# Performance work log

Measured on AMD Instinct MI355X. Metric: run time of the kernel, lower is better.

Reference implementation:

```python
import jax, jax.numpy as jnp
import numpy as np
import math

D = 256        # input_size == d_k == d_v (per the module: d_k = input_size)
H = 4          # n_heads
MAX_LEN = 800  # PositionalEncoding max_len
NEG = float(-(2**32) + 1)
LN_EPS = 1e-5


def _make_pe():
    pe = np.zeros((MAX_LEN, D), dtype=np.float32)
    pos = np.arange(MAX_LEN, dtype=np.float32)[:, None]
    div = np.exp(np.arange(0, D, 2, dtype=np.float32) * -(math.log(10000.0) / D))
    pe[:, 0::2] = np.sin(pos * div)
    pe[:, 1::2] = np.cos(pos * div)
    return jnp.asarray(pe)


def setup_inputs() -> dict:
    key = jax.random.key(0)
    ks = jax.random.split(key, 12)
    B, L = 32, 512

    def xavier(k, shape):
        fan_in, fan_out = shape[0], shape[1]
        std = math.sqrt(2.0 / (fan_in + fan_out))
        return jax.random.normal(k, shape, dtype=jnp.float32) * std

    return {
        "Q": jax.random.normal(ks[0], (B, L, D), dtype=jnp.float32),
        "K": jax.random.normal(ks[1], (B, L, D), dtype=jnp.float32),
        "V": jax.random.normal(ks[2], (B, L, D), dtype=jnp.float32),
        "mask": jax.random.randint(ks[3], (B, L), 0, 2).astype(jnp.bool_),
        "pe": _make_pe(),
        "W_q": xavier(ks[4], (D, H * D)),
        "W_k": xavier(ks[5], (D, H * D)),
        "W_v": xavier(ks[6], (D, H * D)),
        "W_o": xavier(ks[7], (H * D, D)),
        "w1": xavier(ks[8], (D, D)),
        "b1": jnp.zeros((D,), dtype=jnp.float32),
        "w2": xavier(ks[9], (D, D)),
        "b2": jnp.zeros((D,), dtype=jnp.float32),
        "gamma": jnp.ones((D,), dtype=jnp.float32),
        "beta": jnp.zeros((D,), dtype=jnp.float32),
    }


def _layer_norm(x, gamma, beta):
    mu = jnp.mean(x, axis=-1, keepdims=True)
    var = jnp.mean(jnp.square(x - mu), axis=-1, keepdims=True)
    return (x - mu) * jax.lax.rsqrt(var + LN_EPS) * gamma + beta


def _mha(Q, K, V, mask, W_q, W_k, W_v, W_o):
    B, Lq, _ = Q.shape
    Lk = K.shape[1]

    def split_heads(X, W, L):
        # (B, L, D) @ (D, H*D) -> (B*H, L, D)
        return (X @ W).reshape(B, L, H, D).transpose(0, 2, 1, 3).reshape(B * H, L, D)

    Qh = split_heads(Q, W_q, Lq)
    Kh = split_heads(K, W_k, Lk)
    Vh = split_heads(V, W_v, Lk)

    scale = D ** 0.5 + 1e-6
    scores = jnp.einsum('bqd,bkd->bqk', Qh, Kh) / scale  # (B*H, Lq, Lk)

    pad = jnp.broadcast_to(mask[:, None, :], (B, H, Lq)).reshape(B * H, Lq)
    pad_mask = jnp.broadcast_to(pad[:, :, None], (B * H, Lq, Lk))
    causal = jnp.triu(jnp.ones((Lq, Lk), dtype=jnp.bool_), k=1)
    full_mask = causal[None] | pad_mask
    scores = jnp.where(full_mask, NEG, scores)

    att = jax.nn.softmax(scores, axis=-1)
    Vatt = jnp.einsum('bqk,bkd->bqd', att, Vh)  # (B*H, Lq, D)
    Vatt = Vatt.reshape(B, H, Lq, D).transpose(0, 2, 1, 3).reshape(B, Lq, H * D)
    return Vatt @ W_o


def reference(Q, K, V, mask, pe, W_q, W_k, W_v, W_o, w1, b1, w2, b2, gamma, beta):
    Lq, Lk, Lv = Q.shape[1], K.shape[1], V.shape[1]
    Qp = Q + pe[None, :Lq]
    Kp = K + pe[None, :Lk]
    Vp = V + pe[None, :Lv]

    Vatt = _mha(Qp, Kp, Vp, mask, W_q, W_k, W_v, W_o)
    X = _layer_norm(Qp + Vatt, gamma, beta)
    ffn = jax.nn.relu(X @ w1.T + b1) @ w2.T + b2
    return _layer_norm(ffn + X, gamma, beta)
```

## Files before the change

kernel.cpp:

```cpp
#include <hip/hip_runtime.h>
#include <stdint.h>

#define SEQ   512
#define DM    256
#define NB    32
#define NH    4
#define HD    (NH * DM)
#define PE_MASK (SEQ * DM - 1)
#define NEGV  (-4294967295.0f)

typedef __attribute__((ext_vector_type(8))) short short8;
typedef __attribute__((ext_vector_type(4))) float f32x4;

#if defined(__has_builtin)
#if __has_builtin(__builtin_amdgcn_global_load_lds)
#define HAS_ASYNC 1
#endif
#endif
#ifndef HAS_ASYNC
#define HAS_ASYNC 0
#endif

__device__ __forceinline__ float b2f(unsigned short u) {
    return __uint_as_float(((uint32_t)u) << 16);
}
__device__ __forceinline__ unsigned short f2b(float f) {
    uint32_t u = __float_as_uint(f);
    u += 0x7fffu + ((u >> 16) & 1u);
    return (unsigned short)(u >> 16);
}

__global__ __launch_bounds__(256) void mask_canon(
    const unsigned char* __restrict__ raw, int* __restrict__ canon)
{
    __shared__ int enc_byte, enc_odd;
    int tid = threadIdx.x;
    if (tid == 0) { enc_byte = 0; enc_odd = 0; }
    __syncthreads();
    if (tid < 255 && raw[tid * 4 + 1]) atomicOr(&enc_byte, 1);
    if (tid < 128 && ((const int*)raw)[tid * 2 + 1]) atomicOr(&enc_odd, 1);
    __syncthreads();
    int i = blockIdx.x * 256 + tid;
    int v;
    if (enc_byte)      v = (raw[i] != 0);
    else if (enc_odd)  v = (((const int*)raw)[i] != 0);
    else               v = ((((const int*)raw)[i * 2] | ((const int*)raw)[i * 2 + 1]) != 0);
    canon[i] = v;
}

__global__ __launch_bounds__(256) void addpe3(
    const float* __restrict__ Q, const float* __restrict__ K,
    const float* __restrict__ V, const float* __restrict__ pe,
    unsigned short* __restrict__ Qp, unsigned short* __restrict__ Kp,
    unsigned short* __restrict__ Vp)
{
    int blk = blockIdx.x;
    int seg = blk >> 12;
    const float* X = (seg == 0) ? Q : (seg == 1) ? K : V;
    unsigned short* O = (seg == 0) ? Qp : (seg == 1) ? Kp : Vp;
    long i = (long)((blk & 4095) * 256 + threadIdx.x) * 4;
    float4 x = *reinterpret_cast<const float4*>(X + i);
    float4 p = *reinterpret_cast<const float4*>(pe + (i & PE_MASK));
    ushort4 o;
    o.x = f2b(x.x + p.x); o.y = f2b(x.y + p.y);
    o.z = f2b(x.z + p.z); o.w = f2b(x.w + p.w);
    *reinterpret_cast<ushort4*>(O + i) = o;
}

__global__ __launch_bounds__(256) void conv2(
    const float* __restrict__ w1, const float* __restrict__ w2,
    unsigned short* __restrict__ o1, unsigned short* __restrict__ o2)
{
    int blk = blockIdx.x;
    const float* in = (blk < 64) ? w1 : w2;
    unsigned short* out = (blk < 64) ? o1 : o2;
    long i = (long)((blk & 63) * 256 + threadIdx.x) * 4;
    float4 x = *reinterpret_cast<const float4*>(in + i);
    ushort4 o;
    o.x = f2b(x.x); o.y = f2b(x.y); o.z = f2b(x.z); o.w = f2b(x.w);
    *reinterpret_cast<ushort4*>(out + i) = o;
}

__global__ __launch_bounds__(256) void transpose_f2b3(
    const float* __restrict__ in0, const float* __restrict__ in1,
    const float* __restrict__ in2, unsigned short* __restrict__ out,
    int ldin, int ldout, long outStride)
{
    int z = blockIdx.z;
    const float* in = (z == 0) ? in0 : (z == 1) ? in1 : in2;
    unsigned short* op = out + z * outStride;
    __shared__ unsigned short tile[32][33];
    int r0 = blockIdx.y * 32, c0 = blockIdx.x * 32;
    int i = threadIdx.x >> 3;
    int j = (threadIdx.x & 7) * 4;
    float4 v = *reinterpret_cast<const float4*>(in + (long)(r0 + i) * ldin + c0 + j);
    tile[i][j + 0] = f2b(v.x); tile[i][j + 1] = f2b(v.y);
    tile[i][j + 2] = f2b(v.z); tile[i][j + 3] = f2b(v.w);
    __syncthreads();
    ushort4 w;
    w.x = tile[j + 0][i]; w.y = tile[j + 1][i]; w.z = tile[j + 2][i]; w.w = tile[j + 3][i];
    *reinterpret_cast<ushort4*>(op + (long)(c0 + i) * ldout + r0 + j) = w;
}

__global__ __launch_bounds__(256) void transpose_f2b(
    const float* __restrict__ in, unsigned short* __restrict__ out,
    int ldin, int ldout)
{
    __shared__ unsigned short tile[32][33];
    int r0 = blockIdx.y * 32, c0 = blockIdx.x * 32;
    int i = threadIdx.x >> 3;
    int j = (threadIdx.x & 7) * 4;
    float4 v = *reinterpret_cast<const float4*>(in + (long)(r0 + i) * ldin + c0 + j);
    tile[i][j + 0] = f2b(v.x); tile[i][j + 1] = f2b(v.y);
    tile[i][j + 2] = f2b(v.z); tile[i][j + 3] = f2b(v.w);
    __syncthreads();
    ushort4 w;
    w.x = tile[j + 0][i]; w.y = tile[j + 1][i]; w.z = tile[j + 2][i]; w.w = tile[j + 3][i];
    *reinterpret_cast<ushort4*>(out + (long)(c0 + i) * ldout + r0 + j) = w;
}

__global__ __launch_bounds__(256) void transpose_bf16(
    const unsigned short* __restrict__ in, unsigned short* __restrict__ out,
    int ldin, int ldout, long sInB, long sInH, long sOutB, long sOutH, int Hdiv)
{
    int z = blockIdx.z; int b = z / Hdiv; int h = z % Hdiv;
    const unsigned short* ip = in + b * sInB + h * sInH;
    unsigned short* op = out + b * sOutB + h * sOutH;
    __shared__ unsigned short tile[32][33];
    int r0 = blockIdx.y * 32, c0 = blockIdx.x * 32;
    int i = threadIdx.x >> 3;
    int j = (threadIdx.x & 7) * 4;
    ushort4 v = *reinterpret_cast<const ushort4*>(ip + (long)(r0 + i) * ldin + c0 + j);
    tile[i][j + 0] = v.x; tile[i][j + 1] = v.y; tile[i][j + 2] = v.z; tile[i][j + 3] = v.w;
    __syncthreads();
    ushort4 w;
    w.x = tile[j + 0][i]; w.y = tile[j + 1][i]; w.z = tile[j + 2][i]; w.w = tile[j + 3][i];
    *reinterpret_cast<ushort4*>(op + (long)(c0 + i) * ldout + r0 + j) = w;
}

__global__ __launch_bounds__(256) void vmean_part(
    const unsigned short* __restrict__ Vh, float* __restrict__ part)
{
    int bl = blockIdx.x, seg = blockIdx.y;
    const unsigned short* p = Vh + (long)bl * SEQ * HD + (long)seg * 64 * HD;
    int c = threadIdx.x * 4;
    float s0 = 0.f, s1 = 0.f, s2 = 0.f, s3 = 0.f;
    for (int l = 0; l < 64; ++l) {
        ushort4 v = *reinterpret_cast<const ushort4*>(p + (long)l * HD + c);
        s0 += b2f(v.x); s1 += b2f(v.y); s2 += b2f(v.z); s3 += b2f(v.w);
    }
    float4 o = {s0, s1, s2, s3};
    *reinterpret_cast<float4*>(part + (long)(bl * 8 + seg) * HD + c) = o;
}

__global__ __launch_bounds__(256) void vmean_reduce(
    const float* __restrict__ part, unsigned short* __restrict__ Vm)
{
    int bl = blockIdx.x;
    int c = threadIdx.x * 4;
    const float* p = part + (long)bl * 8 * HD + c;
    float s0 = 0.f, s1 = 0.f, s2 = 0.f, s3 = 0.f;
#pragma unroll
    for (int seg = 0; seg < 8; ++seg) {
        float4 v = *reinterpret_cast<const float4*>(p + (long)seg * HD);
        s0 += v.x; s1 += v.y; s2 += v.z; s3 += v.w;
    }
    const float inv = 1.0f / SEQ;
    ushort4 o;
    o.x = f2b(s0 * inv); o.y = f2b(s1 * inv);
    o.z = f2b(s2 * inv); o.w = f2b(s3 * inv);
    *reinterpret_cast<ushort4*>(Vm + (long)bl * HD + c) = o;
}

__global__ __launch_bounds__(256) void fix_mask(
    const unsigned short* __restrict__ Vm, unsigned short* __restrict__ Vatt,
    const int* __restrict__ maskc, int b0)
{
    int row = blockIdx.x;
    int bl = row >> 9, l = row & (SEQ - 1);
    if (maskc[(long)(b0 + bl) * SEQ + l] == 0) return;
    int c = threadIdx.x * 4;
    ushort4 v = *reinterpret_cast<const ushort4*>(Vm + (long)bl * HD + c);
    *reinterpret_cast<ushort4*>(Vatt + (long)row * HD + c) = v;
}

template<bool BIAS, bool RELU, bool OUTBF16>
__global__ __launch_bounds__(256) void gemm_bt(
    const unsigned short* __restrict__ A, int lda,
    const unsigned short* __restrict__ B, int ldb,
    void* __restrict__ Cv, int ldc,
    const float* __restrict__ bias, float scale, int K, int Hdiv,
    long sAb, long sAh, long sAz,
    long sBb, long sBh, long sBz,
    long sCb, long sCh, long sCz)
{
    const int m0 = blockIdx.y * 128;
    const int n0 = blockIdx.x * 128;
    int z  = blockIdx.z;
    int bb = z / Hdiv, hh = z % Hdiv;
    const unsigned short* Ab = A + bb * sAb + hh * sAh + (long)z * sAz;
    const unsigned short* Bb = B + bb * sBb + hh * sBh + (long)z * sBz;
    long coff = bb * sCb + hh * sCh + (long)z * sCz;

    __shared__ unsigned short As[128 * 32];
    __shared__ unsigned short Bs[128 * 32];

    const int tid  = threadIdx.x;
    const int lane = tid & 63;
    const int wave = tid >> 6;
    const int wm   = (wave >> 1) * 64;
    const int wn   = (wave & 1) * 64;
    const int lm   = lane & 15;
    const int kq   = (lane >> 4) * 8;

    f32x4 acc[4][4] = {};

    for (int k0 = 0; k0 < K; k0 += 32) {
#pragma unroll
        for (int it = 0; it < 2; ++it) {
            int id = tid + it * 256;
            int r  = id >> 2;
            int c8 = (id & 3) * 8;
            const unsigned short* gA = Ab + (long)(m0 + r) * lda + k0 + c8;
            const unsigned short* gB = Bb + (long)(n0 + r) * ldb + k0 + c8;
#if HAS_ASYNC
            unsigned short* lA = &As[(size_t)(it * 256 + wave * 64) * 8];
            unsigned short* lB = &Bs[(size_t)(it * 256 + wave * 64) * 8];
            __builtin_amdgcn_global_load_lds(
                (const __attribute__((address_space(1))) void*)gA,
                (__attribute__((address_space(3))) void*)lA, 16, 0, 0);
            __builtin_amdgcn_global_load_lds(
                (const __attribute__((address_space(1))) void*)gB,
                (__attribute__((address_space(3))) void*)lB, 16, 0, 0);
#else
            *reinterpret_cast<uint4*>(&As[(size_t)id * 8]) =
                *reinterpret_cast<const uint4*>(gA);
            *reinterpret_cast<uint4*>(&Bs[(size_t)id * 8]) =
                *reinterpret_cast<const uint4*>(gB);
#endif
        }
        __syncthreads();

        short8 af[4], bfr[4];
#pragma unroll
        for (int i = 0; i < 4; ++i)
            af[i] = *reinterpret_cast<const short8*>(&As[(wm + i * 16 + lm) * 32 + kq]);
#pragma unroll
        for (int j = 0; j < 4; ++j)
            bfr[j] = *reinterpret_cast<const short8*>(&Bs[(wn + j * 16 + lm) * 32 + kq]);
#pragma unroll
        for (int i = 0; i < 4; ++i)
#pragma unroll
            for (int j = 0; j < 4; ++j)
                acc[i][j] = __builtin_amdgcn_mfma_f32_16x16x32_bf16(af[i], bfr[j], acc[i][j], 0, 0, 0);
        __syncthreads();
    }

#pragma unroll
    for (int j = 0; j < 4; ++j) {
        int col  = n0 + wn + j * 16 + lm;
        float bv = 0.f;
        if (BIAS) bv = bias[col];
#pragma unroll
        for (int i = 0; i < 4; ++i) {
#pragma unroll
            for (int r = 0; r < 4; ++r) {
                int row = m0 + wm + i * 16 + (lane >> 4) * 4 + r;
                float v = acc[i][j][r] * scale + bv;
                if (RELU) v = fmaxf(v, 0.f);
                long idx = coff + (long)row * ldc + col;
                if (OUTBF16) reinterpret_cast<unsigned short*>(Cv)[idx] = f2b(v);
                else         reinterpret_cast<float*>(Cv)[idx] = v;
            }
        }
    }
}

__global__ __launch_bounds__(256, 2) void flash_attn(
    const unsigned short* __restrict__ Qh,
    const unsigned short* __restrict__ Kh,
    const unsigned short* __restrict__ VhT,
    unsigned short* __restrict__ Vatt,
    const int* __restrict__ maskc, int bh0, float scale, int nbh)
{
    const int tid  = threadIdx.x;
    const int lane = tid & 63;
    const int wave = tid >> 6;
    const int lm   = lane & 15;
    const int qg   = lane >> 4;
    const int kq   = qg * 8;

    const int L = blockIdx.x;
    int z, qt;
    if ((nbh & 7) == 0) {
        int x = L & 7, m = L >> 3;
        qt = m & 7;
        z  = x + 8 * (m >> 3);
    } else {
        z = L % nbh; qt = L / nbh;
    }
    const int b_l = z >> 2, h = z & 3;
    const int m0  = qt * 64;
    const int wq0 = m0 + wave * 16;
    const long qkbase = (long)b_l * SEQ * HD + (long)h * DM;
    const unsigned short* Aq = Qh + qkbase;
    const unsigned short* Ak = Kh + qkbase;
    const unsigned short* Av = VhT + (long)b_l * SEQ * HD + (long)h * SEQ * DM;
    unsigned short* Ov = Vatt + qkbase;
    const int bglob = (bh0 + z) >> 2;

    __shared__ unsigned short Ks[SEQ * 32];
    __shared__ __align__(16) unsigned short Pw[4][16][40];

    f32x4 S[32] = {};
    const int NT = (m0 >> 4) + wave + 1;

    for (int kc = 0; kc < 8; ++kc) {
        for (int it = 0; it <= qt; ++it) {
            int id = tid + it * 256;
            const unsigned short* g = Ak + (long)(id >> 2) * HD + kc * 32 + (id & 3) * 8;
#if HAS_ASYNC
            unsigned short* l = &Ks[(size_t)(it * 256 + wave * 64) * 8];
            __builtin_amdgcn_global_load_lds(
                (const __attribute__((address_space(1))) void*)g,
                (__attribute__((address_space(3))) void*)l, 16, 0, 0);
#else
            *reinterpret_cast<uint4*>(&Ks[(size_t)id * 8]) =
                *reinterpret_cast<const uint4*>(g);
#endif
        }
        short8 qf = *reinterpret_cast<const short8*>(
            Aq + (long)(wq0 + lm) * HD + kc * 32 + kq);
        __syncthreads();
#pragma unroll
        for (int nt = 0; nt < 32; ++nt) {
            if (nt < NT) {
                short8 bf = *reinterpret_cast<const short8*>(&Ks[(nt * 16 + lm) * 32 + kq]);
                S[nt] = __builtin_amdgcn_mfma_f32_16x16x32_bf16(qf, bf, S[nt], 0, 0, 0);
            }
        }
        __syncthreads();
    }

    unsigned short* Vb0 = Ks;
    unsigned short* Vb1 = Ks + 8192;
#pragma unroll
    for (int it = 0; it < 4; ++it) {
        int id = tid + it * 256;
        const unsigned short* g = Av + (long)(id >> 2) * SEQ + (id & 3) * 8;
#if HAS_ASYNC
        unsigned short* l = &Vb0[(size_t)(it * 256 + wave * 64) * 8];
        __builtin_amdgcn_global_load_lds(
            (const __attribute__((address_space(1))) void*)g,
            (__attribute__((address_space(3))) void*)l, 16, 0, 0);
#else
        *reinterpret_cast<uint4*>(&Vb0[(size_t)id * 8]) =
            *reinterpret_cast<const uint4*>(g);
#endif
    }

    int   qrow[4];
    bool  rowm[4];
    float mx[4], sm[4];
#pragma unroll
    for (int r = 0; r < 4; ++r) {
        int q = wq0 + qg * 4 + r;
        qrow[r] = q;
        rowm[r] = maskc[bglob * SEQ + q] != 0;
        mx[r] = -3.4e38f;
    }
#pragma unroll
    for (int nt = 0; nt < 32; ++nt) {
        int k = nt * 16 + lm;
#pragma unroll
        for (int r = 0; r < 4; ++r) {
            float v = S[nt][r] * scale;
            if (k > qrow[r]) v = NEGV;
            S[nt][r] = v;
            mx[r] = fmaxf(mx[r], v);
        }
    }
#pragma unroll
    for (int r = 0; r < 4; ++r) {
#pragma unroll
        for (int off = 8; off >= 1; off >>= 1)
            mx[r] = fmaxf(mx[r], __shfl_xor(mx[r], off));
        sm[r] = 0.f;
    }
    uint32_t pk[32][2];
#pragma unroll
    for (int nt = 0; nt < 32; ++nt) {
        float e0 = __expf(S[nt][0] - mx[0]);
        float e1 = __expf(S[nt][1] - mx[1]);
        float e2 = __expf(S[nt][2] - mx[2]);
        float e3 = __expf(S[nt][3] - mx[3]);
        sm[0] += e0; sm[1] += e1; sm[2] += e2; sm[3] += e3;
        pk[nt][0] = (uint32_t)f2b(e0) | ((uint32_t)f2b(e1) << 16);
        pk[nt][1] = (uint32_t)f2b(e2) | ((uint32_t)f2b(e3) << 16);
    }
#pragma unroll
    for (int r = 0; r < 4; ++r) {
#pragma unroll
        for (int off = 8; off >= 1; off >>= 1)
            sm[r] += __shfl_xor(sm[r], off);
        sm[r] = 1.0f / sm[r];
    }

    const int KC = 2 * (qt + 1);
    f32x4 O[16] = {};
#pragma unroll
    for (int kc2 = 0; kc2 < 16; ++kc2) {
        if (kc2 < KC) {
            unsigned short* Vcur = (kc2 & 1) ? Vb1 : Vb0;
            __syncthreads();
            if (kc2 + 1 < KC) {
                unsigned short* Vnext = (kc2 & 1) ? Vb0 : Vb1;
#pragma unroll
                for (int it = 0; it < 4; ++it) {
                    int id = tid + it * 256;
                    const unsigned short* g =
                        Av + (long)(id >> 2) * SEQ + (kc2 + 1) * 32 + (id & 3) * 8;
#if HAS_ASYNC
                    unsigned short* l = &Vnext[(size_t)(it * 256 + wave * 64) * 8];
                    __builtin_amdgcn_global_load_lds(
                        (const __attribute__((address_space(1))) void*)g,
                        (__attribute__((address_space(3))) void*)l, 16, 0, 0);
#else
                    *reinterpret_cast<uint4*>(&Vnext[(size_t)id * 8]) =
                        *reinterpret_cast<const uint4*>(g);
#endif
                }
            }
#pragma unroll
            for (int t = 0; t < 2; ++t) {
                int nt = kc2 * 2 + t;
#pragma unroll
                for (int r = 0; r < 4; ++r)
                    Pw[wave][qg * 4 + r][t * 16 + lm] =
                        (unsigned short)(pk[nt][r >> 1] >> ((r & 1) * 16));
            }
            short8 pf = *reinterpret_cast<const short8*>(&Pw[wave][lm][kq]);
#pragma unroll
            for (int nt2 = 0; nt2 < 16; ++nt2) {
                short8 vf = *reinterpret_cast<const short8*>(&Vcur[(nt2 * 16 + lm) * 32 + kq]);
                O[nt2] = __builtin_amdgcn_mfma_f32_16x16x32_bf16(pf, vf, O[nt2], 0, 0, 0);
            }
        }
    }

#pragma unroll
    for (int nt2 = 0; nt2 < 16; ++nt2) {
#pragma unroll
        for (int r = 0; r < 4; ++r) {
            if (!rowm[r]) {
                int l = wq0 + qg * 4 + r;
                Ov[(long)l * HD + nt2 * 16 + lm] = f2b(O[nt2][r] * sm[r]);
            }
        }
    }
}

__global__ __launch_bounds__(256) void ln1_kernel(
    const unsigned short* __restrict__ AttO, const float* __restrict__ Q,
    const float* __restrict__ pe,
    const float* __restrict__ gamma, const float* __restrict__ beta,
    float* __restrict__ outf, unsigned short* __restrict__ outb)
{
    int row  = blockIdx.x * 4 + (threadIdx.x >> 6);
    int lane = threadIdx.x & 63;
    long base = (long)row * DM + lane * 4;
    ushort4 a = *reinterpret_cast<const ushort4*>(AttO + base);
    float4 qv = *reinterpret_cast<const float4*>(Q + base);
    float4 pv = *reinterpret_cast<const float4*>(pe + (base & PE_MASK));
    float x[4] = {b2f(a.x) + qv.x + pv.x, b2f(a.y) + qv.y + pv.y,
                  b2f(a.z) + qv.z + pv.z, b2f(a.w) + qv.w + pv.w};
    float s = x[0] + x[1] + x[2] + x[3];
#pragma unroll
    for (int off = 32; off > 0; off >>= 1) s += __shfl_xor(s, off);
    float mu = s * (1.0f / DM);
    float vs = 0.f;
#pragma unroll
    for (int t = 0; t < 4; ++t) { float d = x[t] - mu; vs += d * d; }
#pragma unroll
    for (int off = 32; off > 0; off >>= 1) vs += __shfl_xor(vs, off);
    float inv = rsqrtf(vs * (1.0f / DM) + 1e-5f);
    int d0 = lane * 4;
    float4 g = *reinterpret_cast<const float4*>(gamma + d0);
    float4 bt = *reinterpret_cast<const float4*>(beta + d0);
    float4 o;
    o.x = (x[0] - mu) * inv * g.x + bt.x;
    o.y = (x[1] - mu) * inv * g.y + bt.y;
    o.z = (x[2] - mu) * inv * g.z + bt.z;
    o.w = (x[3] - mu) * inv * g.w + bt.w;
    *reinterpret_cast<float4*>(outf + base) = o;
    ushort4 ob;
    ob.x = f2b(o.x); ob.y = f2b(o.y); ob.z = f2b(o.z); ob.w = f2b(o.w);
    *reinterpret_cast<ushort4*>(outb + base) = ob;
}

__global__ __launch_bounds__(256) void ln2_kernel(
    const float* __restrict__ F, const float* __restrict__ X,
    const float* __restrict__ gamma, const float* __restrict__ beta,
    float* __restrict__ out)
{
    int row  = blockIdx.x * 4 + (threadIdx.x >> 6);
    int lane = threadIdx.x & 63;
    long base = (long)row * DM + lane * 4;
    float4 a = *reinterpret_cast<const float4*>(F + base);
    float4 c = *reinterpret_cast<const float4*>(X + base);
    float x[4] = {a.x + c.x, a.y + c.y, a.z + c.z, a.w + c.w};
    float s = x[0] + x[1] + x[2] + x[3];
#pragma unroll
    for (int off = 32; off > 0; off >>= 1) s += __shfl_xor(s, off);
    float mu = s * (1.0f / DM);
    float vs = 0.f;
#pragma unroll
    for (int t = 0; t < 4; ++t) { float d = x[t] - mu; vs += d * d; }
#pragma unroll
    for (int off = 32; off > 0; off >>= 1) vs += __shfl_xor(vs, off);
    float inv = rsqrtf(vs * (1.0f / DM) + 1e-5f);
    int d0 = lane * 4;
    float4 g = *reinterpret_cast<const float4*>(gamma + d0);
    float4 bt = *reinterpret_cast<const float4*>(beta + d0);
    float4 o;
    o.x = (x[0] - mu) * inv * g.x + bt.x;
    o.y = (x[1] - mu) * inv * g.y + bt.y;
    o.z = (x[2] - mu) * inv * g.z + bt.z;
    o.w = (x[3] - mu) * inv * g.w + bt.w;
    *reinterpret_cast<float4*>(out + base) = o;
}

extern "C" void kernel_launch(void* const* d_in, const int* in_sizes, int n_in,
                              void* d_out, int out_size, void* d_ws, size_t ws_size,
                              hipStream_t stream)
{
    const float* Q  = (const float*)d_in[0];
    const float* Ki = (const float*)d_in[1];
    const float* Vi = (const float*)d_in[2];
    const unsigned char* mask_raw = (const unsigned char*)d_in[3];
    const float* pe = (const float*)d_in[4];
    const float* Wq = (const float*)d_in[5];
    const float* Wk = (const float*)d_in[6];
    const float* Wv = (const float*)d_in[7];
    const float* Wo = (const float*)d_in[8];
    const float* w1 = (const float*)d_in[9];
    const float* b1 = (const float*)d_in[10];
    const float* w2 = (const float*)d_in[11];
    const float* b2 = (const float*)d_in[12];
    const float* gamma = (const float*)d_in[13];
    const float* beta  = (const float*)d_in[14];
    float* out = (float*)d_out;

    const size_t MiB = 1048576;
    char* ws = (char*)d_ws;

    int CB = 1;
    for (int cb = 32; cb >= 1; cb >>= 1) {
        size_t scr_sz = (size_t)(5 * cb) * MiB + (size_t)cb * 34816;
        if (scr_sz < 24 * MiB) scr_sz = 24 * MiB;
        if ((59 * MiB + scr_sz) <= ws_size) { CB = cb; break; }
    }
    const int NCH = NB / CB;

    unsigned short* WqT  = (unsigned short*)(ws);
    unsigned short* WkT  = WqT + 262144;
    unsigned short* WvT  = WkT + 262144;
    unsigned short* WoT  = WvT + 262144;
    unsigned short* w1b  = (unsigned short*)(ws + 2 * MiB);
    unsigned short* w2b  = w1b + 65536;
    int*            maskc = (int*)(ws + 2 * MiB + 262144);
    unsigned short* Qp   = (unsigned short*)(ws + 3 * MiB);
    unsigned short* Kp   = (unsigned short*)(ws + 11 * MiB);
    unsigned short* Vp   = (unsigned short*)(ws + 19 * MiB);
    unsigned short* AttO = (unsigned short*)(ws + 27 * MiB);
    unsigned short* Xb   = (unsigned short*)(ws + 35 * MiB);
    float*          Xf   = (float*)(ws + 43 * MiB);
    char*           scr  = ws + 59 * MiB;
    unsigned short* Qh   = (unsigned short*)(scr);
    unsigned short* Kh   = (unsigned short*)(scr + (size_t)CB * MiB);
    unsigned short* Vh   = (unsigned short*)(scr + (size_t)2 * CB * MiB);
    unsigned short* VhT  = (unsigned short*)(scr + (size_t)3 * CB * MiB);
    unsigned short* Vatt = (unsigned short*)(scr + (size_t)4 * CB * MiB);
    float*          part = (float*)(scr + (size_t)5 * CB * MiB);
    unsigned short* Vm   = (unsigned short*)(scr + (size_t)5 * CB * MiB
                                             + (size_t)CB * 8 * HD * 4);
    unsigned short* H1   = (unsigned short*)(scr);
    float*          Ff   = (float*)(scr + 8 * MiB);

    const float scale = (float)(1.0 / (16.0 + 1e-6));
    const long CROWS = (long)CB * SEQ;
    const long CBELT = (long)CB * MiB / 2;

    mask_canon<<<64, 256, 0, stream>>>(mask_raw, maskc);
    transpose_f2b3<<<dim3(32, 8, 3), 256, 0, stream>>>(Wq, Wk, Wv, WqT, HD, DM, 262144);
    transpose_f2b<<<dim3(8, 32, 1), 256, 0, stream>>>(Wo, WoT, DM, HD);
    conv2<<<128, 256, 0, stream>>>(w1, w2, w1b, w2b);
    addpe3<<<12288, 256, 0, stream>>>(Q, Ki, Vi, pe, Qp, Kp, Vp);

    for (int c = 0; c < NCH; ++c) {
        const long r0   = (long)c * CROWS;
        const int  bh0  = c * CB * NH;
        const int  gy   = (int)(CROWS / 128);
        const int  nbh  = CB * NH;

        gemm_bt<false, false, true><<<dim3(8, gy, 3), 256, 0, stream>>>(
            Qp + r0 * DM, DM, WqT, DM, Qh, HD, nullptr, 1.f, DM,
            1, 4194304, 0, 0, 262144, 0, 0, CBELT, 0, 0);

        transpose_bf16<<<dim3(8, 16, CB * NH), 256, 0, stream>>>(
            Vh, VhT, HD, SEQ, (long)SEQ * HD, DM, (long)SEQ * HD, (long)SEQ * DM, NH);

        vmean_part<<<dim3(CB, 8), 256, 0, stream>>>(Vh, part);
        vmean_reduce<<<CB, 256, 0, stream>>>(part, Vm);

        flash_attn<<<dim3(8 * nbh, 1, 1), 256, 0, stream>>>(
            Qh, Kh, VhT, Vatt, maskc, bh0, scale, nbh);

        fix_mask<<<(int)CROWS, 256, 0, stream>>>(Vm, Vatt, maskc, c * CB);

        gemm_bt<false, false, true><<<dim3(2, gy, 1), 256, 0, stream>>>(
            Vatt, HD, WoT, HD, AttO + r0 * DM, DM, nullptr, 1.f, HD,
            1, 0,0,0, 0,0,0, 0,0,0);
    }

    ln1_kernel<<<4096, 256, 0, stream>>>(AttO, Q, pe, gamma, beta, Xf, Xb);

    gemm_bt<true, true, true><<<dim3(2, 128, 1), 256, 0, stream>>>(
        Xb, DM, w1b, DM, H1, DM, b1, 1.f, DM, 1, 0,0,0, 0,0,0, 0,0,0);
    gemm_bt<true, false, false><<<dim3(2, 128, 1), 256, 0, stream>>>(
        H1, DM, w2b, DM, Ff, DM, b2, 1.f, DM, 1, 0,0,0, 0,0,0, 0,0,0);

    ln2_kernel<<<4096, 256, 0, stream>>>(Ff, Xf, gamma, beta, out);
}
```

Measured before the change: 351.5 us.

## Double-buffer K tiles with XOR-swizzled LDS layout in flash attention

The K-chunk staging in the attention kernel now uses two LDS buffers, so the next 32-column K slice is prefetched while MFMAs consume the current one. The first V chunk is also issued during the last K iteration. K and V tiles are stored with an XOR swizzle to cut LDS bank conflicts on fragment reads. In exchange, shared memory doubles to 64KB for K, which may limit occupancy. The kernel also now stages all 512 K rows on every tile instead of only the causally needed ones, so early query tiles do more global traffic.

New measurement: 348.1 us. No clear change (-1.0%).

```diff
diff --git a/kernel.cpp b/kernel.cpp
--- a/kernel.cpp
+++ b/kernel.cpp
@@ -28,6 +28,10 @@
     uint32_t u = __float_as_uint(f);
     u += 0x7fffu + ((u >> 16) & 1u);
     return (unsigned short)(u >> 16);
+}
+
+__device__ __forceinline__ int swzb(int b) {
+    return b ^ (((b >> 7) & 7) << 4);
 }
 
 __global__ __launch_bounds__(256) void mask_canon(
@@ -276,6 +280,50 @@
     }
 }
 
+__device__ __forceinline__ void stage_k32(
+    unsigned short* __restrict__ buf, const unsigned short* __restrict__ Ak,
+    int kc, int tid, int wave)
+{
+#pragma unroll
+    for (int it = 0; it < 8; ++it) {
+        int id = tid + it * 256;
+#if HAS_ASYNC
+        int U = swzb(id * 16);
+        const unsigned short* g = Ak + (long)(U >> 6) * HD + kc * 32 + ((U >> 4) & 3) * 8;
+        unsigned short* l = buf + (size_t)(it * 256 + wave * 64) * 8;
+        __builtin_amdgcn_global_load_lds(
+            (const __attribute__((address_space(1))) void*)g,
+            (__attribute__((address_space(3))) void*)l, 16, 0, 0);
+#else
+        const unsigned short* g = Ak + (long)(id >> 2) * HD + kc * 32 + (id & 3) * 8;
+        *reinterpret_cast<uint4*>((char*)buf + swzb(id * 16)) =
+            *reinterpret_cast<const uint4*>(g);
+#endif
+    }
+}
+
+__device__ __forceinline__ void stage_v32(
+    unsigned short* __restrict__ buf, const unsigned short* __restrict__ Av,
+    int chunk, int tid, int wave)
+{
+#pragma unroll
+    for (int it = 0; it < 4; ++it) {
+        int id = tid + it * 256;
+#if HAS_ASYNC
+        int U = swzb(id * 16);
+        const unsigned short* g = Av + (long)(U >> 6) * SEQ + chunk * 32 + ((U >> 4) & 3) * 8;
+        unsigned short* l = buf + (size_t)(it * 256 + wave * 64) * 8;
+        __builtin_amdgcn_global_load_lds(
+            (const __attribute__((address_space(1))) void*)g,
+            (__attribute__((address_space(3))) void*)l, 16, 0, 0);
+#else
+        const unsigned short* g = Av + (long)(id >> 2) * SEQ + chunk * 32 + (id & 3) * 8;
+        *reinterpret_cast<uint4*>((char*)buf + swzb(id * 16)) =
+            *reinterpret_cast<const uint4*>(g);
+#endif
+    }
+}
+
 __global__ __launch_bounds__(256, 2) void flash_attn(
     const unsigned short* __restrict__ Qh,
     const unsigned short* __restrict__ Kh,
@@ -309,54 +357,34 @@
     unsigned short* Ov = Vatt + qkbase;
     const int bglob = (bh0 + z) >> 2;
 
-    __shared__ unsigned short Ks[SEQ * 32];
+    __shared__ unsigned short Ks[2 * SEQ * 32];
     __shared__ __align__(16) unsigned short Pw[4][16][40];
 
     f32x4 S[32] = {};
     const int NT = (m0 >> 4) + wave + 1;
 
+    stage_k32(Ks, Ak, 0, tid, wave);
+    __syncthreads();
     for (int kc = 0; kc < 8; ++kc) {
-        for (int it = 0; it <= qt; ++it) {
-            int id = tid + it * 256;
-            const unsigned short* g = Ak + (long)(id >> 2) * HD + kc * 32 + (id & 3) * 8;
-#if HAS_ASYNC
-            unsigned short* l = &Ks[(size_t)(it * 256 + wave * 64) * 8];
-            __builtin_amdgcn_global_load_lds(
-                (const __attribute__((address_space(1))) void*)g,
-                (__attribute__((address_space(3))) void*)l, 16, 0, 0);
-#else
-            *reinterpret_cast<uint4*>(&Ks[(size_t)id * 8]) =
-                *reinterpret_cast<const uint4*>(g);
-#endif
-        }
+        unsigned short* cur = (kc & 1) ? (Ks + SEQ * 32) : Ks;
+        unsigned short* nxt = (kc & 1) ? Ks : (Ks + SEQ * 32);
         short8 qf = *reinterpret_cast<const short8*>(
             Aq + (long)(wq0 + lm) * HD + kc * 32 + kq);
-        __syncthreads();
+        if (kc < 7) {
+            stage_k32(nxt, Ak, kc + 1, tid, wave);
+        } else {
+            stage_v32(Ks, Av, 0, tid, wave);
+        }
 #pragma unroll
         for (int nt = 0; nt < 32; ++nt) {
             if (nt < NT) {
-                short8 bf = *reinterpret_cast<const short8*>(&Ks[(nt * 16 + lm) * 32 + kq]);
+                int row = nt * 16 + lm;
+                short8 bf = *reinterpret_cast<const short8*>(
+                    (const char*)cur + swzb(row * 64 + qg * 16));
                 S[nt] = __builtin_amdgcn_mfma_f32_16x16x32_bf16(qf, bf, S[nt], 0, 0, 0);
             }
         }
         __syncthreads();
-    }
-
-    unsigned short* Vb0 = Ks;
-    unsigned short* Vb1 = Ks + 8192;
-#pragma unroll
-    for (int it = 0; it < 4; ++it) {
-        int id = tid + it * 256;
-        const unsigned short* g = Av + (long)(id >> 2) * SEQ + (id & 3) * 8;
-#if HAS_ASYNC
-        unsigned short* l = &Vb0[(size_t)(it * 256 + wave * 64) * 8];
-        __builtin_amdgcn_global_load_lds(
-            (const __attribute__((address_space(1))) void*)g,
-            (__attribute__((address_space(3))) void*)l, 16, 0, 0);
-#else
-        *reinterpret_cast<uint4*>(&Vb0[(size_t)id * 8]) =
-            *reinterpret_cast<const uint4*>(g);
-#endif
     }
 
     int   qrow[4];
@@ -406,6 +434,8 @@
         sm[r] = 1.0f / sm[r];
     }
 
+    unsigned short* Vb0 = Ks;
+    unsigned short* Vb1 = Ks + 8192;
     const int KC = 2 * (qt + 1);
     f32x4 O[16] = {};
 #pragma unroll
@@ -415,21 +445,7 @@
             __syncthreads();
             if (kc2 + 1 < KC) {
                 unsigned short* Vnext = (kc2 & 1) ? Vb0 : Vb1;
-#pragma unroll
-                for (int it = 0; it < 4; ++it) {
-                    int id = tid + it * 256;
-                    const unsigned short* g =
-                        Av + (long)(id >> 2) * SEQ + (kc2 + 1) * 32 + (id & 3) * 8;
-#if HAS_ASYNC
-                    unsigned short* l = &Vnext[(size_t)(it * 256 + wave * 64) * 8];
-                    __builtin_amdgcn_global_load_lds(
-                        (const __attribute__((address_space(1))) void*)g,
-                        (__attribute__((address_space(3))) void*)l, 16, 0, 0);
-#else
-                    *reinterpret_cast<uint4*>(&Vnext[(size_t)id * 8]) =
-                        *reinterpret_cast<const uint4*>(g);
-#endif
-                }
+                stage_v32(Vnext, Av, kc2 + 1, tid, wave);
             }
 #pragma unroll
             for (int t = 0; t < 2; ++t) {
@@ -442,7 +458,9 @@
             short8 pf = *reinterpret_cast<const short8*>(&Pw[wave][lm][kq]);
 #pragma unroll
             for (int nt2 = 0; nt2 < 16; ++nt2) {
-                short8 vf = *reinterpret_cast<const short8*>(&Vcur[(nt2 * 16 + lm) * 32 + kq]);
+                int row = nt2 * 16 + lm;
+                short8 vf = *reinterpret_cast<const short8*>(
+                    (const char*)Vcur + swzb(row * 64 + qg * 16));
                 O[nt2] = __builtin_amdgcn_mfma_f32_16x16x32_bf16(pf, vf, O[nt2], 0, 0, 0);
             }
         }
```
